# Kernel tuning notes

Hardware: AMD Instinct MI355X
Metric: run time of the kernel (lower is better)

Reference implementation:

```python
import jax, jax.numpy as jnp
import numpy as np

B, N, C, H = 4, 1024, 256, 8
HD = C // H
SCALE = HD ** -0.5


def setup_inputs() -> dict:
    key = jax.random.key(0)
    ks = jax.random.split(key, 8)
    x = jax.random.normal(ks[0], (B, N, C), jnp.float32)
    voxel_coord = jax.random.uniform(ks[1], (B, N, 3), jnp.float32)
    # Linear weights stored as [in, out] so y = x @ W + b (same math as torch x @ W.T)
    W_qk = jax.random.normal(ks[2], (C, 2 * C), jnp.float32) * 0.02
    W_v = jax.random.normal(ks[3], (C, C), jnp.float32) * 0.02
    W_proj = jax.random.normal(ks[4], (C, C), jnp.float32) * 0.02
    b_proj = jnp.zeros((C,), jnp.float32)
    W_pos = jax.random.normal(ks[5], (4, H), jnp.float32) * 0.02
    b_pos = jnp.zeros((H,), jnp.float32)
    gating = jnp.ones((H,), jnp.float32)
    return dict(x=x, voxel_coord=voxel_coord, W_qk=W_qk, W_v=W_v,
                W_proj=W_proj, b_proj=b_proj, W_pos=W_pos, b_pos=b_pos,
                gating=gating)


def reference(x, voxel_coord, W_qk, W_v, W_proj, b_proj, W_pos, b_pos, gating):
    b, n, c = x.shape
    # Relative 3D positional encoding: positions[b,i,j] = p[j] - p[i]; feature = [dx,dy,dz,dist]
    diff = voxel_coord[:, None, :, :] - voxel_coord[:, :, None, :]          # [B,N,N,3]
    dist = jnp.sqrt(jnp.sum(diff * diff, axis=-1, keepdims=True))           # [B,N,N,1]
    rel = jnp.concatenate([diff, dist], axis=-1)                            # [B,N,N,4]

    # Positional score per head, softmax over keys j
    pos_logits = jnp.einsum('bijf,fh->bhij', rel, W_pos) + b_pos[None, :, None, None]
    pos_score = jax.nn.softmax(pos_logits, axis=-1)                         # [B,H,N,N]

    # Content score: SDPA with V = I  ==  plain softmax attention matrix
    qk = (x @ W_qk).reshape(b, n, 2, H, HD)
    q = jnp.transpose(qk[:, :, 0], (0, 2, 1, 3))                            # [B,H,N,hd]
    k = jnp.transpose(qk[:, :, 1], (0, 2, 1, 3))
    patch_score = jax.nn.softmax(jnp.einsum('bhid,bhjd->bhij', q, k) * SCALE, axis=-1)

    # Gated mix + renormalize
    sig = jax.nn.sigmoid(gating)[None, :, None, None]
    attn = (1.0 - sig) * patch_score + sig * pos_score
    attn = attn / jnp.sum(attn, axis=-1, keepdims=True)

    v = (x @ W_v).reshape(b, n, H, HD).transpose(0, 2, 1, 3)                # [B,H,N,hd]
    out = jnp.einsum('bhij,bhjd->bihd', attn, v).reshape(b, n, c)           # [B,N,C]
    out = out @ W_proj + b_proj
    return out
```

## Files before the change

kernel.cpp:

```cpp
#include <hip/hip_runtime.h>

#define LOG2E 1.4426950408889634f

typedef __attribute__((ext_vector_type(8))) short bf16x8_t;
typedef __attribute__((ext_vector_type(4))) float f32x4_t;

#if __has_builtin(__builtin_amdgcn_exp2f)
#define EXP2F_(x) __builtin_amdgcn_exp2f(x)
#else
__device__ __forceinline__ float EXP2F_(float x) {
    float r; asm volatile("v_exp_f32 %0, %1\ns_nop 1" : "=v"(r) : "v"(x)); return r;
}
#endif
#if __has_builtin(__builtin_amdgcn_sqrtf)
#define SQRTF_(x) __builtin_amdgcn_sqrtf(x)
#else
__device__ __forceinline__ float SQRTF_(float x) {
    float r; asm volatile("v_sqrt_f32 %0, %1\ns_nop 1" : "=v"(r) : "v"(x)); return r;
}
#endif

__device__ __forceinline__ unsigned short f2bf(float f) {
    unsigned u = __float_as_uint(f);
    u += 0x7fffu + ((u >> 16) & 1u);
    return (unsigned short)(u >> 16);
}

__global__ __launch_bounds__(256) void k_convert(
    const float* __restrict__ x, const float* __restrict__ Wqk,
    const float* __restrict__ Wv, const float* __restrict__ Wpj,
    unsigned short* __restrict__ x_bf, unsigned short* __restrict__ Wqk_t,
    unsigned short* __restrict__ Wv_t, unsigned short* __restrict__ Wp_t)
{
    __shared__ unsigned short T[64 * 72];
    const int bid = blockIdx.x, tid = threadIdx.x;
    if (bid < 64) {
        const float* src; unsigned short* dst; int N_, kt, nt;
        if (bid < 32)      { src = Wqk; dst = Wqk_t; N_ = 512; kt = bid & 3; nt = bid >> 2; }
        else if (bid < 48) { int t = bid - 32; src = Wv;  dst = Wv_t; N_ = 256; kt = t & 3; nt = t >> 2; }
        else               { int t = bid - 48; src = Wpj; dst = Wp_t; N_ = 256; kt = t & 3; nt = t >> 2; }
        const int kr = tid >> 2, seg = tid & 3;
        #pragma unroll
        for (int u = 0; u < 4; ++u) {
            float4 v = *(const float4*)(src + (kt * 64 + kr) * N_ + nt * 64 + seg * 16 + u * 4);
            T[(seg * 16 + u * 4 + 0) * 72 + kr] = f2bf(v.x);
            T[(seg * 16 + u * 4 + 1) * 72 + kr] = f2bf(v.y);
            T[(seg * 16 + u * 4 + 2) * 72 + kr] = f2bf(v.z);
            T[(seg * 16 + u * 4 + 3) * 72 + kr] = f2bf(v.w);
        }
        __syncthreads();
        const int n = tid >> 2, s2 = tid & 3;
        uint4 a = *(uint4*)&T[n * 72 + s2 * 16];
        uint4 b2 = *(uint4*)&T[n * 72 + s2 * 16 + 8];
        *(uint4*)(dst + (nt * 64 + n) * 256 + kt * 64 + s2 * 16) = a;
        *(uint4*)(dst + (nt * 64 + n) * 256 + kt * 64 + s2 * 16 + 8) = b2;
    } else {
        const int cb2 = bid - 64;
        const float4* xs = (const float4*)x + (size_t)cb2 * 8192;
        uint2* xd = (uint2*)x_bf + (size_t)cb2 * 8192;
        for (int i = tid; i < 8192; i += 256) {
            float4 v = xs[i];
            uint2 o;
            o.x = (unsigned)f2bf(v.x) | ((unsigned)f2bf(v.y) << 16);
            o.y = (unsigned)f2bf(v.z) | ((unsigned)f2bf(v.w) << 16);
            xd[i] = o;
        }
    }
}

__global__ __launch_bounds__(256) void k_qkv(
    const unsigned short* __restrict__ x_bf,
    const unsigned short* __restrict__ Wqk_t,
    const unsigned short* __restrict__ Wv_t,
    unsigned short* __restrict__ q_ws, unsigned short* __restrict__ k_ws,
    unsigned short* __restrict__ v_ws)
{
    __shared__ unsigned short Al[64 * 72];
    __shared__ unsigned short Bl[64 * 72];
    const int tid = threadIdx.x;
    const int n0 = blockIdx.x * 64;
    const int row0 = blockIdx.y * 64;
    const int w = tid >> 6, lane = tid & 63;
    const int lhi = lane >> 4, llo = lane & 15;

    f32x4_t acc[4] = {};
    for (int kc = 0; kc < 4; ++kc) {
        int idx = tid;
        #pragma unroll
        for (int s = 0; s < 2; ++s, idx += 256) {
            int r = idx >> 3, c8 = idx & 7;
            *(uint4*)(&Al[r * 72 + c8 * 8]) =
                *(const uint4*)(x_bf + (row0 + r) * 256 + kc * 64 + c8 * 8);
        }
        idx = tid;
        #pragma unroll
        for (int s = 0; s < 2; ++s, idx += 256) {
            int r = idx >> 3, c8 = idx & 7;
            int ng = n0 + r;
            const unsigned short* src = (ng < 512) ? (Wqk_t + ng * 256) : (Wv_t + (ng - 512) * 256);
            *(uint4*)(&Bl[r * 72 + c8 * 8]) = *(const uint4*)(src + kc * 64 + c8 * 8);
        }
        __syncthreads();
        #pragma unroll
        for (int ks = 0; ks < 2; ++ks) {
            bf16x8_t a = *(const bf16x8_t*)(&Al[(w * 16 + llo) * 72 + ks * 32 + lhi * 8]);
            #pragma unroll
            for (int nt = 0; nt < 4; ++nt) {
                bf16x8_t b = *(const bf16x8_t*)(&Bl[(nt * 16 + llo) * 72 + ks * 32 + lhi * 8]);
                acc[nt] = __builtin_amdgcn_mfma_f32_16x16x32_bf16(a, b, acc[nt], 0, 0, 0);
            }
        }
        __syncthreads();
    }
    constexpr float QSC = (float)(1.4426950408889634 / 5.656854249492380195206754896838);
    #pragma unroll
    for (int nt = 0; nt < 4; ++nt) {
        int ng = n0 + nt * 16 + llo;
        #pragma unroll
        for (int r = 0; r < 4; ++r) {
            int ig = row0 + w * 16 + lhi * 4 + r;
            float val = acc[nt][r];
            int b = ig >> 10, i = ig & 1023;
            if (ng < 256) {
                int h = ng >> 5, d = ng & 31;
                q_ws[((b * 8 + h) * 1024 + i) * 32 + d] = f2bf(val * QSC);
            } else if (ng < 512) {
                int c = ng - 256, h = c >> 5, d = c & 31;
                k_ws[((b * 8 + h) * 1024 + i) * 32 + d] = f2bf(val);
            } else {
                int c = ng - 512, h = c >> 5, d = c & 31;
                v_ws[((b * 8 + h) * 1024 + i) * 32 + d] = f2bf(val);
            }
        }
    }
}

__global__ __launch_bounds__(256) void k_attn(
    const unsigned short* __restrict__ q_ws,
    const unsigned short* __restrict__ k_ws,
    const unsigned short* __restrict__ v_ws,
    const float* __restrict__ coords,
    const float* __restrict__ W_pos,
    const float* __restrict__ b_pos,
    float* __restrict__ part)
{
    __shared__ unsigned short Kl[64 * 40];
    __shared__ unsigned short Vt[32 * 72];
    __shared__ unsigned short Wp[64 * 72];
    __shared__ unsigned short Wq[64 * 72];

    const int tid = threadIdx.x;
    const int bid = blockIdx.x;
    const int xcd = bid & 7, idx = bid >> 3;
    const int bh = xcd * 4 + (idx >> 5);
    const int rem = idx & 31;
    const int it = rem >> 1;
    const int jh = rem & 1;
    const int b = bh >> 3, h = bh & 7;

    const int w = tid >> 6, lane = tid & 63;
    const int lhi = lane >> 4, llo = lane & 15;

    const float wx = W_pos[0 * 8 + h] * LOG2E;
    const float wy = W_pos[1 * 8 + h] * LOG2E;
    const float wz = W_pos[2 * 8 + h] * LOG2E;
    const float wd = W_pos[3 * 8 + h] * LOG2E;
    const float bp = b_pos[h] * LOG2E;

    const int i_base = it * 64 + w * 16;
    bf16x8_t qf = *(const bf16x8_t*)(q_ws + (bh * 1024 + i_base + llo) * 32 + lhi * 8);

    const float* cb_ = coords + b * 3072;
    float pix[4], piy[4], piz[4];
    #pragma unroll
    for (int r = 0; r < 4; ++r) {
        int i = i_base + lhi * 4 + r;
        pix[r] = cb_[i * 3 + 0]; piy[r] = cb_[i * 3 + 1]; piz[r] = cb_[i * 3 + 2];
    }

    bf16x8_t ones;
    #pragma unroll
    for (int e = 0; e < 8; ++e) ones[e] = (short)0x3F80;

    f32x4_t accP[2] = {}, accQ[2] = {};
    f32x4_t accLp = {}, accLq = {};

    for (int t = 0; t < 8; ++t) {
        const int j0 = jh * 512 + t * 64;
        {
            int r = tid >> 2, c = tid & 3;
            *(uint4*)(&Kl[r * 40 + c * 8]) =
                *(const uint4*)(k_ws + (bh * 1024 + j0 + r) * 32 + c * 8);
            uint4 vv = *(const uint4*)(v_ws + (bh * 1024 + j0 + lane) * 32 + w * 8);
            const unsigned short* pv = (const unsigned short*)&vv;
            #pragma unroll
            for (int e = 0; e < 8; ++e) Vt[(w * 8 + e) * 72 + lane] = pv[e];
        }
        __syncthreads();

        #pragma unroll
        for (int jq = 0; jq < 4; ++jq) {
            bf16x8_t kf = *(const bf16x8_t*)(&Kl[(jq * 16 + llo) * 40 + lhi * 8]);
            f32x4_t zero = {};
            f32x4_t sv = __builtin_amdgcn_mfma_f32_16x16x32_bf16(qf, kf, zero, 0, 0, 0);
            int jg = j0 + jq * 16 + llo;
            float pjx = cb_[jg * 3 + 0], pjy = cb_[jg * 3 + 1], pjz = cb_[jg * 3 + 2];
            #pragma unroll
            for (int r = 0; r < 4; ++r) {
                float dx = pjx - pix[r], dy = pjy - piy[r], dz = pjz - piz[r];
                float d2 = fmaf(dx, dx, fmaf(dy, dy, dz * dz));
                float dist = SQRTF_(d2);
                float spos = fmaf(wd, dist, fmaf(wz, dz, fmaf(wy, dy, fmaf(wx, dx, bp))));
                float ep = EXP2F_(sv[r]);
                float eq = EXP2F_(spos);
                int ib = w * 16 + lhi * 4 + r;
                Wp[ib * 72 + jq * 16 + llo] = f2bf(ep);
                Wq[ib * 72 + jq * 16 + llo] = f2bf(eq);
            }
        }

        #pragma unroll
        for (int jb = 0; jb < 2; ++jb) {
            bf16x8_t bP = *(const bf16x8_t*)(&Wp[(w * 16 + llo) * 72 + jb * 32 + lhi * 8]);
            bf16x8_t bQ = *(const bf16x8_t*)(&Wq[(w * 16 + llo) * 72 + jb * 32 + lhi * 8]);
            accLp = __builtin_amdgcn_mfma_f32_16x16x32_bf16(ones, bP, accLp, 0, 0, 0);
            accLq = __builtin_amdgcn_mfma_f32_16x16x32_bf16(ones, bQ, accLq, 0, 0, 0);
            #pragma unroll
            for (int dt = 0; dt < 2; ++dt) {
                bf16x8_t af = *(const bf16x8_t*)(&Vt[(dt * 16 + llo) * 72 + jb * 32 + lhi * 8]);
                accP[dt] = __builtin_amdgcn_mfma_f32_16x16x32_bf16(af, bP, accP[dt], 0, 0, 0);
                accQ[dt] = __builtin_amdgcn_mfma_f32_16x16x32_bf16(af, bQ, accQ[dt], 0, 0, 0);
            }
        }
        __syncthreads();
    }

    float* pb = part + (size_t)((bh * 16 + it) * 2 + jh) * 4224;
    #pragma unroll
    for (int dt = 0; dt < 2; ++dt) {
        #pragma unroll
        for (int r = 0; r < 4; ++r) {
            int d = dt * 16 + lhi * 4 + r;
            pb[d * 64 + w * 16 + llo] = accP[dt][r];
            pb[2048 + d * 64 + w * 16 + llo] = accQ[dt][r];
        }
    }
    if (lane < 16) {
        pb[4096 + w * 16 + lane] = accLp[0];
        pb[4160 + w * 16 + lane] = accLq[0];
    }
}

__global__ __launch_bounds__(256) void k_comb(
    const float* __restrict__ part, const float* __restrict__ gating,
    unsigned short* __restrict__ o_ws)
{
    const int bid = blockIdx.x;
    const int bh = bid >> 4, it = bid & 15;
    const int b = bh >> 3, h = bh & 7;
    const int tid = threadIdx.x, w = tid >> 6, i = tid & 63;
    const float* p0 = part + (size_t)(bid * 2) * 4224;
    const float* p1 = p0 + 4224;
    float sig = 1.0f / (1.0f + __expf(-gating[h]));
    float Lp = p0[4096 + i] + p1[4096 + i];
    float Lq = p0[4160 + i] + p1[4160 + i];
    float ca = (1.0f - sig) / Lp, cb2 = sig / Lq;
    unsigned short ob[8];
    #pragma unroll
    for (int e = 0; e < 8; ++e) {
        int d = w * 8 + e;
        float Op = p0[d * 64 + i] + p1[d * 64 + i];
        float Oq = p0[2048 + d * 64 + i] + p1[2048 + d * 64 + i];
        ob[e] = f2bf(ca * Op + cb2 * Oq);
    }
    *(uint4*)(o_ws + ((size_t)(b * 1024 + it * 64 + i)) * 256 + h * 32 + w * 8) = *(uint4*)ob;
}

__global__ __launch_bounds__(256) void k_proj(
    const unsigned short* __restrict__ A,
    const unsigned short* __restrict__ Bt,
    const float* __restrict__ bias,
    float* __restrict__ out)
{
    __shared__ unsigned short Al[64 * 72];
    __shared__ unsigned short Bl[64 * 72];
    const int tid = threadIdx.x;
    const int n0 = blockIdx.x * 64;
    const int row0 = blockIdx.y * 64;
    const int w = tid >> 6, lane = tid & 63;
    const int lhi = lane >> 4, llo = lane & 15;

    f32x4_t acc[4] = {};
    for (int kc = 0; kc < 4; ++kc) {
        int idx = tid;
        #pragma unroll
        for (int s = 0; s < 2; ++s, idx += 256) {
            int r = idx >> 3, c8 = idx & 7;
            *(uint4*)(&Al[r * 72 + c8 * 8]) =
                *(const uint4*)(A + (row0 + r) * 256 + kc * 64 + c8 * 8);
        }
        idx = tid;
        #pragma unroll
        for (int s = 0; s < 2; ++s, idx += 256) {
            int r = idx >> 3, c8 = idx & 7;
            *(uint4*)(&Bl[r * 72 + c8 * 8]) =
                *(const uint4*)(Bt + (n0 + r) * 256 + kc * 64 + c8 * 8);
        }
        __syncthreads();
        #pragma unroll
        for (int ks = 0; ks < 2; ++ks) {
            bf16x8_t a = *(const bf16x8_t*)(&Al[(w * 16 + llo) * 72 + ks * 32 + lhi * 8]);
            #pragma unroll
            for (int nt = 0; nt < 4; ++nt) {
                bf16x8_t b = *(const bf16x8_t*)(&Bl[(nt * 16 + llo) * 72 + ks * 32 + lhi * 8]);
                acc[nt] = __builtin_amdgcn_mfma_f32_16x16x32_bf16(a, b, acc[nt], 0, 0, 0);
            }
        }
        __syncthreads();
    }
    #pragma unroll
    for (int nt = 0; nt < 4; ++nt) {
        int ng = n0 + nt * 16 + llo;
        float bv = bias[ng];
        #pragma unroll
        for (int r = 0; r < 4; ++r) {
            int ig = row0 + w * 16 + lhi * 4 + r;
            out[ig * 256 + ng] = acc[nt][r] + bv;
        }
    }
}

extern "C" void kernel_launch(void* const* d_in, const int* in_sizes, int n_in,
                              void* d_out, int out_size, void* d_ws, size_t ws_size,
                              hipStream_t stream)
{
    const float* x    = (const float*)d_in[0];
    const float* vc   = (const float*)d_in[1];
    const float* Wqk  = (const float*)d_in[2];
    const float* Wv   = (const float*)d_in[3];
    const float* Wpj  = (const float*)d_in[4];
    const float* bpj  = (const float*)d_in[5];
    const float* Wpos = (const float*)d_in[6];
    const float* bpos = (const float*)d_in[7];
    const float* gat  = (const float*)d_in[8];
    float* out = (float*)d_out;

    char* ws = (char*)d_ws;
    unsigned short* x_bf  = (unsigned short*)(ws + 0);
    unsigned short* Wqk_t = (unsigned short*)(ws + 2097152);
    unsigned short* Wv_t  = (unsigned short*)(ws + 2359296);
    unsigned short* Wp_t  = (unsigned short*)(ws + 2490368);
    unsigned short* q_ws  = (unsigned short*)(ws + 2621440);
    unsigned short* k_ws  = (unsigned short*)(ws + 4718592);
    unsigned short* v_ws  = (unsigned short*)(ws + 6815744);
    unsigned short* o_ws  = (unsigned short*)(ws + 8912896);
    float*          partf = (float*)(ws + 11010048);

    hipLaunchKernelGGL(k_convert, dim3(96), dim3(256), 0, stream,
                       x, Wqk, Wv, Wpj, x_bf, Wqk_t, Wv_t, Wp_t);
    hipLaunchKernelGGL(k_qkv, dim3(12, 64), dim3(256), 0, stream,
                       x_bf, Wqk_t, Wv_t, q_ws, k_ws, v_ws);
    hipLaunchKernelGGL(k_attn, dim3(1024), dim3(256), 0, stream,
                       q_ws, k_ws, v_ws, vc, Wpos, bpos, partf);
    hipLaunchKernelGGL(k_comb, dim3(512), dim3(256), 0, stream,
                       partf, gat, o_ws);
    hipLaunchKernelGGL(k_proj, dim3(4, 64), dim3(256), 0, stream,
                       o_ws, Wp_t, bpj, out);
}
```

Before: 133.0 us.

## Use direct global-to-LDS loads with swizzle and precompute per-key position terms

```diff
diff --git a/kernel.cpp b/kernel.cpp
--- a/kernel.cpp
+++ b/kernel.cpp
@@ -1,4 +1,5 @@
 #include <hip/hip_runtime.h>
+#include <hip/hip_bf16.h>
 
 #define LOG2E 1.4426950408889634f
 
@@ -24,6 +25,21 @@
     unsigned u = __float_as_uint(f);
     u += 0x7fffu + ((u >> 16) & 1u);
     return (unsigned short)(u >> 16);
+}
+
+__device__ __forceinline__ unsigned pk2(float lo, float hi) {
+    union { __hip_bfloat162 h2; unsigned u; } cvt;
+    cvt.h2 = __float22bfloat162_rn(make_float2(lo, hi));
+    return cvt.u;
+}
+
+__device__ __forceinline__ void stage16(const unsigned short* g, unsigned short* l, int lane) {
+#if __has_builtin(__builtin_amdgcn_global_load_lds)
+    __builtin_amdgcn_global_load_lds((const __attribute__((address_space(1))) void*)g,
+                                     (__attribute__((address_space(3))) void*)l, 16, 0, 0);
+#else
+    *(uint4*)((char*)l + lane * 16) = *(const uint4*)g;
+#endif
 }
 
 __global__ __launch_bounds__(256) void k_convert(
@@ -75,38 +91,35 @@
     unsigned short* __restrict__ q_ws, unsigned short* __restrict__ k_ws,
     unsigned short* __restrict__ v_ws)
 {
-    __shared__ unsigned short Al[64 * 72];
-    __shared__ unsigned short Bl[64 * 72];
+    __shared__ unsigned short Al[64 * 64];
+    __shared__ unsigned short Bl[64 * 64];
     const int tid = threadIdx.x;
     const int n0 = blockIdx.x * 64;
     const int row0 = blockIdx.y * 64;
     const int w = tid >> 6, lane = tid & 63;
     const int lhi = lane >> 4, llo = lane & 15;
+    const unsigned short* Bsrc = (n0 < 512) ? (Wqk_t + n0 * 256) : (Wv_t + (n0 - 512) * 256);
+
+    const int sr = lane >> 3, sc = lane & 7;
+    const int scx = sc ^ (sr & 7);
 
     f32x4_t acc[4] = {};
     for (int kc = 0; kc < 4; ++kc) {
-        int idx = tid;
-        #pragma unroll
-        for (int s = 0; s < 2; ++s, idx += 256) {
-            int r = idx >> 3, c8 = idx & 7;
-            *(uint4*)(&Al[r * 72 + c8 * 8]) =
-                *(const uint4*)(x_bf + (row0 + r) * 256 + kc * 64 + c8 * 8);
-        }
-        idx = tid;
-        #pragma unroll
-        for (int s = 0; s < 2; ++s, idx += 256) {
-            int r = idx >> 3, c8 = idx & 7;
-            int ng = n0 + r;
-            const unsigned short* src = (ng < 512) ? (Wqk_t + ng * 256) : (Wv_t + (ng - 512) * 256);
-            *(uint4*)(&Bl[r * 72 + c8 * 8]) = *(const uint4*)(src + kc * 64 + c8 * 8);
+        #pragma unroll
+        for (int s = 0; s < 2; ++s) {
+            int chunk = w * 2 + s;
+            int r = chunk * 8 + sr;
+            stage16(x_bf + (row0 + r) * 256 + kc * 64 + scx * 8, &Al[chunk * 512], lane);
+            stage16(Bsrc + r * 256 + kc * 64 + scx * 8, &Bl[chunk * 512], lane);
         }
         __syncthreads();
         #pragma unroll
         for (int ks = 0; ks < 2; ++ks) {
-            bf16x8_t a = *(const bf16x8_t*)(&Al[(w * 16 + llo) * 72 + ks * 32 + lhi * 8]);
+            int ua = ((ks * 4 + lhi) ^ (llo & 7)) * 8;
+            bf16x8_t a = *(const bf16x8_t*)(&Al[(w * 16 + llo) * 64 + ua]);
             #pragma unroll
             for (int nt = 0; nt < 4; ++nt) {
-                bf16x8_t b = *(const bf16x8_t*)(&Bl[(nt * 16 + llo) * 72 + ks * 32 + lhi * 8]);
+                bf16x8_t b = *(const bf16x8_t*)(&Bl[(nt * 16 + llo) * 64 + ua]);
                 acc[nt] = __builtin_amdgcn_mfma_f32_16x16x32_bf16(a, b, acc[nt], 0, 0, 0);
             }
         }
@@ -144,10 +157,12 @@
     const float* __restrict__ b_pos,
     float* __restrict__ part)
 {
-    __shared__ unsigned short Kl[64 * 40];
+    __shared__ unsigned short Kl[64 * 32];
     __shared__ unsigned short Vt[32 * 72];
     __shared__ unsigned short Wp[64 * 72];
     __shared__ unsigned short Wq[64 * 72];
+    __shared__ float4 XYZS[512];
+    __shared__ float  AJ[512];
 
     const int tid = threadIdx.x;
     const int bid = blockIdx.x;
@@ -161,21 +176,26 @@
     const int w = tid >> 6, lane = tid & 63;
     const int lhi = lane >> 4, llo = lane & 15;
 
-    const float wx = W_pos[0 * 8 + h] * LOG2E;
-    const float wy = W_pos[1 * 8 + h] * LOG2E;
-    const float wz = W_pos[2 * 8 + h] * LOG2E;
-    const float wd = W_pos[3 * 8 + h] * LOG2E;
-    const float bp = b_pos[h] * LOG2E;
+    const float wxl = W_pos[0 * 8 + h] * LOG2E;
+    const float wyl = W_pos[1 * 8 + h] * LOG2E;
+    const float wzl = W_pos[2 * 8 + h] * LOG2E;
+    const float wdl = W_pos[3 * 8 + h] * LOG2E;
+    const float bpl = b_pos[h] * LOG2E;
 
     const int i_base = it * 64 + w * 16;
     bf16x8_t qf = *(const bf16x8_t*)(q_ws + (bh * 1024 + i_base + llo) * 32 + lhi * 8);
 
     const float* cb_ = coords + b * 3072;
-    float pix[4], piy[4], piz[4];
-    #pragma unroll
-    for (int r = 0; r < 4; ++r) {
-        int i = i_base + lhi * 4 + r;
-        pix[r] = cb_[i * 3 + 0]; piy[r] = cb_[i * 3 + 1]; piz[r] = cb_[i * 3 + 2];
+    const int ig = i_base + llo;
+    float xi = cb_[ig * 3 + 0], yi = cb_[ig * 3 + 1], zi = cb_[ig * 3 + 2];
+    float si = fmaf(xi, xi, fmaf(yi, yi, zi * zi));
+    float cil = fmaf(wzl, zi, fmaf(wyl, yi, wxl * xi));
+
+    for (int jl = tid; jl < 512; jl += 256) {
+        int jg = jh * 512 + jl;
+        float xj = cb_[jg * 3 + 0], yj = cb_[jg * 3 + 1], zj = cb_[jg * 3 + 2];
+        XYZS[jl] = make_float4(xj, yj, zj, fmaf(xj, xj, fmaf(yj, yj, zj * zj)));
+        AJ[jl] = fmaf(wzl, zj, fmaf(wyl, yj, wxl * xj)) + bpl;
     }
 
     bf16x8_t ones;
@@ -185,12 +205,16 @@
     f32x4_t accP[2] = {}, accQ[2] = {};
     f32x4_t accLp = {}, accLq = {};
 
+    const int ksr = lane >> 2, ksc = lane & 3;
+    const int kscx = ksc ^ (ksr & 3);
+    __syncthreads();
+
     for (int t = 0; t < 8; ++t) {
         const int j0 = jh * 512 + t * 64;
+        const int jlb0 = t * 64;
         {
-            int r = tid >> 2, c = tid & 3;
-            *(uint4*)(&Kl[r * 40 + c * 8]) =
-                *(const uint4*)(k_ws + (bh * 1024 + j0 + r) * 32 + c * 8);
+            int r = w * 16 + ksr;
+            stage16(k_ws + (bh * 1024 + j0 + r) * 32 + kscx * 8, &Kl[w * 512], lane);
             uint4 vv = *(const uint4*)(v_ws + (bh * 1024 + j0 + lane) * 32 + w * 8);
             const unsigned short* pv = (const unsigned short*)&vv;
             #pragma unroll
@@ -200,23 +224,29 @@
 
         #pragma unroll
         for (int jq = 0; jq < 4; ++jq) {
-            bf16x8_t kf = *(const bf16x8_t*)(&Kl[(jq * 16 + llo) * 40 + lhi * 8]);
+            int krow = jq * 16 + llo;
+            bf16x8_t kf = *(const bf16x8_t*)(&Kl[krow * 32 + ((lhi ^ (krow & 3)) * 8)]);
             f32x4_t zero = {};
-            f32x4_t sv = __builtin_amdgcn_mfma_f32_16x16x32_bf16(qf, kf, zero, 0, 0, 0);
-            int jg = j0 + jq * 16 + llo;
-            float pjx = cb_[jg * 3 + 0], pjy = cb_[jg * 3 + 1], pjz = cb_[jg * 3 + 2];
+            f32x4_t sv = __builtin_amdgcn_mfma_f32_16x16x32_bf16(kf, qf, zero, 0, 0, 0);
+            int jlb = jlb0 + jq * 16 + lhi * 4;
+            float ep[4], eq[4];
             #pragma unroll
             for (int r = 0; r < 4; ++r) {
-                float dx = pjx - pix[r], dy = pjy - piy[r], dz = pjz - piz[r];
-                float d2 = fmaf(dx, dx, fmaf(dy, dy, dz * dz));
+                float4 cj = XYZS[jlb + r];
+                float aj = AJ[jlb + r];
+                float dot = fmaf(cj.x, xi, fmaf(cj.y, yi, cj.z * zi));
+                float d2 = fmaf(-2.0f, dot, si + cj.w);
                 float dist = SQRTF_(d2);
-                float spos = fmaf(wd, dist, fmaf(wz, dz, fmaf(wy, dy, fmaf(wx, dx, bp))));
-                float ep = EXP2F_(sv[r]);
-                float eq = EXP2F_(spos);
-                int ib = w * 16 + lhi * 4 + r;
-                Wp[ib * 72 + jq * 16 + llo] = f2bf(ep);
-                Wq[ib * 72 + jq * 16 + llo] = f2bf(eq);
-            }
+                float spos = fmaf(wdl, dist, aj - cil);
+                ep[r] = EXP2F_(sv[r]);
+                eq[r] = EXP2F_(spos);
+            }
+            uint2 wpP, wpQ;
+            wpP.x = pk2(ep[0], ep[1]); wpP.y = pk2(ep[2], ep[3]);
+            wpQ.x = pk2(eq[0], eq[1]); wpQ.y = pk2(eq[2], eq[3]);
+            int off = (w * 16 + llo) * 72 + jq * 16 + lhi * 4;
+            *(uint2*)(&Wp[off]) = wpP;
+            *(uint2*)(&Wq[off]) = wpQ;
         }
 
         #pragma unroll
@@ -282,37 +312,33 @@
     const float* __restrict__ bias,
     float* __restrict__ out)
 {
-    __shared__ unsigned short Al[64 * 72];
-    __shared__ unsigned short Bl[64 * 72];
+    __shared__ unsigned short Al[64 * 64];
+    __shared__ unsigned short Bl[64 * 64];
     const int tid = threadIdx.x;
     const int n0 = blockIdx.x * 64;
     const int row0 = blockIdx.y * 64;
     const int w = tid >> 6, lane = tid & 63;
     const int lhi = lane >> 4, llo = lane & 15;
+    const int sr = lane >> 3, sc = lane & 7;
+    const int scx = sc ^ (sr & 7);
 
     f32x4_t acc[4] = {};
     for (int kc = 0; kc < 4; ++kc) {
-        int idx = tid;
-        #pragma unroll
-        for (int s = 0; s < 2; ++s, idx += 256) {
-            int r = idx >> 3, c8 = idx & 7;
-            *(uint4*)(&Al[r * 72 + c8 * 8]) =
-                *(const uint4*)(A + (row0 + r) * 256 + kc * 64 + c8 * 8);
-        }
-        idx = tid;
-        #pragma unroll
-        for (int s = 0; s < 2; ++s, idx += 256) {
-            int r = idx >> 3, c8 = idx & 7;
-            *(uint4*)(&Bl[r * 72 + c8 * 8]) =
-                *(const uint4*)(Bt + (n0 + r) * 256 + kc * 64 + c8 * 8);
+        #pragma unroll
+        for (int s = 0; s < 2; ++s) {
+            int chunk = w * 2 + s;
+            int r = chunk * 8 + sr;
+            stage16(A + (row0 + r) * 256 + kc * 64 + scx * 8, &Al[chunk * 512], lane);
+            stage16(Bt + (n0 + r) * 256 + kc * 64 + scx * 8, &Bl[chunk * 512], lane);
         }
         __syncthreads();
         #pragma unroll
         for (int ks = 0; ks < 2; ++ks) {
-            bf16x8_t a = *(const bf16x8_t*)(&Al[(w * 16 + llo) * 72 + ks * 32 + lhi * 8]);
+            int ua = ((ks * 4 + lhi) ^ (llo & 7)) * 8;
+            bf16x8_t a = *(const bf16x8_t*)(&Al[(w * 16 + llo) * 64 + ua]);
             #pragma unroll
             for (int nt = 0; nt < 4; ++nt) {
-                bf16x8_t b = *(const bf16x8_t*)(&Bl[(nt * 16 + llo) * 72 + ks * 32 + lhi * 8]);
+                bf16x8_t b = *(const bf16x8_t*)(&Bl[(nt * 16 + llo) * 64 + ua]);
                 acc[nt] = __builtin_amdgcn_mfma_f32_16x16x32_bf16(a, b, acc[nt], 0, 0, 0);
             }
         }
```

After: 125.7 us. 5.5% less time.
